# Kernel tuning notes

Hardware: AMD Instinct MI355X
Metric: run time of the kernel (lower is better)

## Reference

```python
import jax, jax.numpy as jnp
import numpy as np

L, D, H, F, NB = 6, 1024, 16, 4096, 33  # layers, d_model, heads, ffn_hidden, rel buckets
DH = D // H
B, S = 4, 1024


def _ln(x, g, b):
    m = x.mean(-1, keepdims=True)
    v = ((x - m) ** 2).mean(-1, keepdims=True)
    return (x - m) * jax.lax.rsqrt(v + 1e-6) * g + b


def setup_inputs() -> dict:
    key = jax.random.key(0)
    ks = iter(jax.random.split(key, 16))
    nrm = lambda shape, s: jax.random.normal(next(ks), shape, jnp.float32) * s
    w = 0.02
    return {
        "x": jax.random.normal(next(ks), (B, S, D), jnp.float32),
        "relative_ids": jax.random.randint(next(ks), (S, S), 0, NB, jnp.int32),
        "Wq": nrm((L, D, D), w), "bq": jnp.zeros((L, D)),
        "Wk": nrm((L, D, D), w), "bk": jnp.zeros((L, D)),
        "Wv": nrm((L, D, D), w), "bv": jnp.zeros((L, D)),
        "Wo": nrm((L, D, D), w), "bo": jnp.zeros((L, D)),
        "Erel": nrm((L, NB, DH), w),          # relative key embeddings (rel-e)
        "Brel": nrm((L, H, NB), w),           # relative bias per head (rel-b)
        "g1": jnp.ones((L, D)), "be1": jnp.zeros((L, D)),
        "g2": jnp.ones((L, D)), "be2": jnp.zeros((L, D)),
        "W1": nrm((L, D, F), w), "b1": jnp.zeros((L, F)),
        "W2": nrm((L, F, D), w), "b2": jnp.zeros((L, D)),
    }


def reference(x, relative_ids, Wq, bq, Wk, bk, Wv, bv, Wo, bo, Erel, Brel,
              g1, be1, g2, be2, W1, b1, W2, b2):
    scale = 1.0 / np.sqrt(DH).astype(np.float32)
    for l in range(L):
        # --- relative-position MHA (rel-eb) ---
        q = (x @ Wq[l] + bq[l]).reshape(B, S, H, DH).transpose(0, 2, 1, 3)
        k = (x @ Wk[l] + bk[l]).reshape(B, S, H, DH).transpose(0, 2, 1, 3)
        v = (x @ Wv[l] + bv[l]).reshape(B, S, H, DH).transpose(0, 2, 1, 3)
        scores = jnp.einsum('bhqd,bhkd->bhqk', q, k)
        e = Erel[l][relative_ids]                      # [S,S,DH]
        scores = scores + jnp.einsum('bhqd,qkd->bhqk', q, e)
        scores = scores + Brel[l][:, relative_ids][None]  # [1,H,S,S]
        attn = jax.nn.softmax(scores * scale, axis=-1)
        a = jnp.einsum('bhqk,bhkd->bqhd', attn, v).reshape(B, S, D)
        a = a @ Wo[l] + bo[l]
        # dropout p=0.1 is identity in eval mode
        ff_in = _ln(x + a, g1[l], be1[l])
        ff = jax.nn.relu(ff_in @ W1[l] + b1[l]) @ W2[l] + b2[l]
        x = _ln(ff_in + ff, g2[l], be2[l])
    return x
```

## Files before the change

kernel.cpp:

```cpp
#include <hip/hip_runtime.h>

typedef __attribute__((ext_vector_type(8))) short short8;
typedef __attribute__((ext_vector_type(4))) float f32x4;
typedef __attribute__((ext_vector_type(4))) unsigned short ushort4v;

#define AS1(p) ((const __attribute__((address_space(1))) void*)(p))
#define AS3(p) ((__attribute__((address_space(3))) void*)(p))

__device__ __forceinline__ float bf2f(unsigned short v) {
    union { unsigned u; float f; } c; c.u = ((unsigned)v) << 16; return c.f;
}
__device__ __forceinline__ unsigned short f2bf(float f) {
    union { float f; unsigned u; } c; c.f = f;
    unsigned u = c.u;
    return (unsigned short)((u + 0x7FFFu + ((u >> 16) & 1u)) >> 16);
}

__global__ __launch_bounds__(256) void transpose_cvt(
    const float* __restrict__ in, unsigned short* __restrict__ out, int R, int C)
{
    __shared__ float tile[64][68];
    int bx = blockIdx.x * 64;
    int by = blockIdx.y * 64;
    int tx = threadIdx.x & 15, ty = threadIdx.x >> 4;
    #pragma unroll
    for (int i = 0; i < 4; i++) {
        int r = ty + i * 16;
        f32x4 v = *(const f32x4*)(in + (size_t)(by + r) * C + bx + tx * 4);
        *(f32x4*)&tile[r][tx * 4] = v;
    }
    __syncthreads();
    #pragma unroll
    for (int i = 0; i < 4; i++) {
        int c = ty + i * 16;
        ushort4v o = { f2bf(tile[tx * 4 + 0][c]), f2bf(tile[tx * 4 + 1][c]),
                       f2bf(tile[tx * 4 + 2][c]), f2bf(tile[tx * 4 + 3][c]) };
        *(ushort4v*)(out + (size_t)(bx + c) * R + by + tx * 4) = o;
    }
}

__global__ __launch_bounds__(256) void cvt_f32_bf16(
    const float* __restrict__ in, unsigned short* __restrict__ out, int n)
{
    int i4 = (blockIdx.x * 256 + threadIdx.x) * 4;
    if (i4 < n) {
        f32x4 v = *(const f32x4*)(in + i4);
        ushort4v o = { f2bf(v[0]), f2bf(v[1]), f2bf(v[2]), f2bf(v[3]) };
        *(ushort4v*)(out + i4) = o;
    }
}

__global__ __launch_bounds__(256) void transpose_v(
    const unsigned short* __restrict__ in, unsigned short* __restrict__ out)
{
    __shared__ unsigned short t[64][66];
    int bh = blockIdx.y, s0 = blockIdx.x * 64;
    int tid = threadIdx.x;
    int r = tid >> 2, c = (tid & 3) * 16;
    const unsigned short* ip = in + ((size_t)bh * 1024 + s0 + r) * 64 + c;
    short8 a0 = *(const short8*)ip;
    short8 a1 = *(const short8*)(ip + 8);
    #pragma unroll
    for (int i = 0; i < 8; i++) t[r][c + i] = (unsigned short)a0[i];
    #pragma unroll
    for (int i = 0; i < 8; i++) t[r][c + 8 + i] = (unsigned short)a1[i];
    __syncthreads();
    int d = tid >> 2, sc = (tid & 3) * 16;
    short8 v0, v1;
    #pragma unroll
    for (int i = 0; i < 8; i++) v0[i] = (short)t[sc + i][d];
    #pragma unroll
    for (int i = 0; i < 8; i++) v1[i] = (short)t[sc + 8 + i][d];
    unsigned short* op = out + ((size_t)bh * 64 + d) * 1024 + s0 + sc;
    *(short8*)op = v0;
    *(short8*)(op + 8) = v1;
}

template <int MODE>
__global__ __launch_bounds__(256)
void gemm_bt(const unsigned short* __restrict__ A,
             const unsigned short* __restrict__ Bt,
             const float* __restrict__ bias0,
             const float* __restrict__ bias1,
             const float* __restrict__ bias2,
             float* __restrict__ outF0,
             float* __restrict__ outF1,
             float* __restrict__ outF2,
             float* __restrict__ outF3,
             unsigned short* __restrict__ outB,
             int M, int N, int K, int Kc)
{
    __shared__ __align__(16) unsigned short As[2][128 * 32];
    __shared__ __align__(16) unsigned short Bs[2][128 * 32];

    int tid = threadIdx.x;
    int wave = tid >> 6, lane = tid & 63;
    int ml = lane & 15, quad = lane >> 4;

    int nx = gridDim.x, ny = gridDim.y;
    int nwg = nx * ny;
    int lin = blockIdx.x + nx * (blockIdx.y + ny * blockIdx.z);
    int total = nwg * gridDim.z;
    int cpx = total >> 3;
    int logical = (lin & 7) * cpx + (lin >> 3);
    int z = logical / nwg;
    int rem = logical - z * nwg;
    int m0 = (rem / nx) * 128, n0 = (rem % nx) * 128;

    int wm = (wave >> 1) * 64, wn = (wave & 1) * 64;

    f32x4 acc[4][4];
    #pragma unroll
    for (int i = 0; i < 4; i++)
        #pragma unroll
        for (int j = 0; j < 4; j++)
            #pragma unroll
            for (int r = 0; r < 4; r++) acc[i][j][r] = 0.0f;

    int srow = lane >> 2, skp = (lane & 3) * 8;
    int kbeg = z * Kc;
    int nt = Kc >> 5;

    auto stage = [&](int buf, int k0) {
        #pragma unroll
        for (int c2 = 0; c2 < 2; c2++) {
            int c = wave + c2 * 4;
            const unsigned short* ga = A + (size_t)(m0 + c * 16 + srow) * K + (k0 + skp);
            __builtin_amdgcn_global_load_lds(AS1(ga), AS3(&As[buf][c * 512]), 16, 0, 0);
            const unsigned short* gb = Bt + (size_t)(n0 + c * 16 + srow) * K + (k0 + skp);
            __builtin_amdgcn_global_load_lds(AS1(gb), AS3(&Bs[buf][c * 512]), 16, 0, 0);
        }
    };

    stage(0, kbeg);
    __syncthreads();

    for (int t = 0; t < nt; t++) {
        int cur = t & 1;
        if (t + 1 < nt) stage(cur ^ 1, kbeg + (t + 1) * 32);

        short8 af[4], bfr[4];
        #pragma unroll
        for (int i = 0; i < 4; i++)
            af[i] = *(const short8*)(&As[cur][(wm + i * 16 + ml) * 32 + quad * 8]);
        #pragma unroll
        for (int j = 0; j < 4; j++)
            bfr[j] = *(const short8*)(&Bs[cur][(wn + j * 16 + ml) * 32 + quad * 8]);
        #pragma unroll
        for (int i = 0; i < 4; i++)
            #pragma unroll
            for (int j = 0; j < 4; j++)
                acc[i][j] = __builtin_amdgcn_mfma_f32_16x16x32_bf16(af[i], bfr[j], acc[i][j], 0, 0, 0);

        if (t + 1 < nt) __syncthreads();
    }

    float* outF = (z == 0) ? outF0 : (z == 1) ? outF1 : (z == 2) ? outF2 : outF3;

    size_t Ns = (size_t)N;
    #pragma unroll
    for (int j = 0; j < 4; j++) {
        int ng = n0 + wn + j * 16 + ml;
        float bv;
        if (MODE == 2) {
            int which = ng >> 10;
            const float* bp = (which == 0) ? bias0 : ((which == 1) ? bias1 : bias2);
            bv = bp[ng & 1023];
        } else {
            bv = (z == 0) ? bias0[ng] : 0.0f;
        }
        #pragma unroll
        for (int i = 0; i < 4; i++) {
            #pragma unroll
            for (int r = 0; r < 4; r++) {
                int mg = m0 + wm + i * 16 + quad * 4 + r;
                float v = acc[i][j][r] + bv;
                if (MODE == 0) {
                    outF[(size_t)mg * Ns + ng] = v;
                } else if (MODE == 1) {
                    outB[(size_t)mg * Ns + ng] = f2bf(fmaxf(v, 0.0f));
                } else {
                    int which = ng >> 10, wi = ng & 1023;
                    int h = wi >> 6, d = wi & 63;
                    int b = mg >> 10, s = mg & 1023;
                    outB[(size_t)which * 4194304 +
                         ((size_t)(b * 16 + h) * 1024 + s) * 64 + d] = f2bf(v);
                }
            }
        }
    }
}

__global__ __launch_bounds__(256) void qe_kernel(
    const unsigned short* __restrict__ q,
    const float* __restrict__ Erel,
    const float* __restrict__ Brel,
    float* __restrict__ out)
{
    int idx = blockIdx.x * 256 + threadIdx.x;
    if (idx >= 2162688) return;
    int n = idx % 33;
    int row = idx / 33;
    const short8* qv = (const short8*)(q + (size_t)row * 64);
    float s = 0.0f;
    #pragma unroll
    for (int c = 0; c < 8; c++) {
        short8 qq = qv[c];
        const float* e = Erel + n * 64 + c * 8;
        #pragma unroll
        for (int j = 0; j < 8; j++) s += bf2f((unsigned short)qq[j]) * e[j];
    }
    int h = (row >> 10) & 15;
    out[idx] = (s + Brel[h * 33 + n]) * 0.125f;
}

__global__ __launch_bounds__(256, 3)
void attn_kernel(const unsigned short* __restrict__ Q,
                 const unsigned short* __restrict__ Kin,
                 const unsigned short* __restrict__ Vt,
                 const int* __restrict__ rid,
                 const float* __restrict__ qEc,
                 unsigned short* __restrict__ outp)
{
    const float scale = 0.125f;
    int bid = blockIdx.x;
    int bh = bid & 63, qt = bid >> 6;
    int b = bh >> 4, h = bh & 15;
    int q0 = qt * 64;
    size_t bhs = (size_t)bh;

    __shared__ __align__(16) unsigned short Ks[64 * 72];
    __shared__ __align__(16) unsigned short VT[64 * 72];
    __shared__ __align__(16) unsigned short Ps[4][16 * 72];
    __shared__ float combS[4][528];

    int tid = threadIdx.x;
    int wave = tid >> 6, lane = tid & 63;
    int ml = lane & 15, quad = lane >> 4;

    const unsigned short* Qp = Q + (bhs * 1024 + q0) * 64;
    const unsigned short* Kp = Kin + bhs * 65536;
    const unsigned short* Vp = Vt + bhs * 65536;

    short8 aq0 = *(const short8*)(Qp + (size_t)(wave * 16 + ml) * 64 + quad * 8);
    short8 aq1 = *(const short8*)(Qp + (size_t)(wave * 16 + ml) * 64 + 32 + quad * 8);

    {
        const float* qEw = qEc + (bhs * 1024 + q0 + wave * 16) * 33;
        for (int i = lane; i < 528; i += 64) combS[wave][i] = qEw[i];
    }

    int srow = tid >> 2, scol = (tid & 3) * 16;
    const unsigned short* Kg = Kp + (size_t)srow * 64 + scol;
    const unsigned short* Vg = Vp + (size_t)srow * 1024 + scol;
    const int* ridBase = rid + (size_t)(q0 + wave * 16 + quad * 4) * 1024;

    float m_st[4], l_st[4];
    f32x4 o_acc[4];
    #pragma unroll
    for (int r = 0; r < 4; r++) { m_st[r] = -1e30f; l_st[r] = 0.0f; }
    #pragma unroll
    for (int j = 0; j < 4; j++)
        #pragma unroll
        for (int r = 0; r < 4; r++) o_acc[j][r] = 0.0f;

    short8 pk0 = *(const short8*)(Kg);
    short8 pk1 = *(const short8*)(Kg + 8);
    short8 pv0 = *(const short8*)(Vg);
    short8 pv1 = *(const short8*)(Vg + 8);

    for (int kt = 0; kt < 16; kt++) {
        if (kt > 0) __syncthreads();
        *(short8*)(Ks + srow * 72 + scol)     = pk0;
        *(short8*)(Ks + srow * 72 + scol + 8) = pk1;
        *(short8*)(VT + srow * 72 + scol)     = pv0;
        *(short8*)(VT + srow * 72 + scol + 8) = pv1;
        __syncthreads();

        if (kt + 1 < 16) {
            pk0 = *(const short8*)(Kg + (kt + 1) * 4096);
            pk1 = *(const short8*)(Kg + (kt + 1) * 4096 + 8);
            pv0 = *(const short8*)(Vg + (kt + 1) * 64);
            pv1 = *(const short8*)(Vg + (kt + 1) * 64 + 8);
        }

        int rv[4][4];
        #pragma unroll
        for (int r = 0; r < 4; r++) {
            const int* rp = ridBase + (size_t)r * 1024 + kt * 64 + ml;
            #pragma unroll
            for (int j = 0; j < 4; j++) rv[r][j] = rp[j * 16];
        }

        f32x4 s_acc[4];
        #pragma unroll
        for (int j = 0; j < 4; j++)
            #pragma unroll
            for (int r = 0; r < 4; r++) s_acc[j][r] = 0.0f;
        __builtin_amdgcn_s_setprio(1);
        #pragma unroll
        for (int j = 0; j < 4; j++) {
            short8 bk0 = *(const short8*)(Ks + (j * 16 + ml) * 72 + quad * 8);
            short8 bk1 = *(const short8*)(Ks + (j * 16 + ml) * 72 + 32 + quad * 8);
            s_acc[j] = __builtin_amdgcn_mfma_f32_16x16x32_bf16(aq0, bk0, s_acc[j], 0, 0, 0);
            s_acc[j] = __builtin_amdgcn_mfma_f32_16x16x32_bf16(aq1, bk1, s_acc[j], 0, 0, 0);
        }
        __builtin_amdgcn_s_setprio(0);

        float mxl[4];
        #pragma unroll
        for (int r = 0; r < 4; r++) {
            int rl = quad * 4 + r;
            #pragma unroll
            for (int j = 0; j < 4; j++)
                s_acc[j][r] = s_acc[j][r] * scale + combS[wave][rl * 33 + rv[r][j]];
            mxl[r] = fmaxf(fmaxf(s_acc[0][r], s_acc[1][r]), fmaxf(s_acc[2][r], s_acc[3][r]));
        }

        bool ok = (mxl[0] <= m_st[0] + 8.0f) & (mxl[1] <= m_st[1] + 8.0f)
                & (mxl[2] <= m_st[2] + 8.0f) & (mxl[3] <= m_st[3] + 8.0f);
        if (__all(ok)) {
            #pragma unroll
            for (int r = 0; r < 4; r++) {
                int rl = quad * 4 + r;
                float ps = 0.0f;
                #pragma unroll
                for (int j = 0; j < 4; j++) {
                    float pv = __expf(s_acc[j][r] - m_st[r]);
                    ps += pv;
                    Ps[wave][rl * 72 + j * 16 + ml] = f2bf(pv);
                }
                l_st[r] += ps;
            }
        } else {
            #pragma unroll
            for (int r = 0; r < 4; r++) {
                int rl = quad * 4 + r;
                float m0 = mxl[r];
                m0 = fmaxf(m0, __shfl_xor(m0, 1, 64));
                m0 = fmaxf(m0, __shfl_xor(m0, 2, 64));
                m0 = fmaxf(m0, __shfl_xor(m0, 4, 64));
                m0 = fmaxf(m0, __shfl_xor(m0, 8, 64));
                float mnew = fmaxf(m_st[r], m0);
                float alpha = __expf(m_st[r] - mnew);
                float ps = 0.0f;
                #pragma unroll
                for (int j = 0; j < 4; j++) {
                    float pv = __expf(s_acc[j][r] - mnew);
                    ps += pv;
                    Ps[wave][rl * 72 + j * 16 + ml] = f2bf(pv);
                }
                l_st[r] = l_st[r] * alpha + ps;
                m_st[r] = mnew;
                #pragma unroll
                for (int j = 0; j < 4; j++) o_acc[j][r] *= alpha;
            }
        }

        short8 ap0 = *(const short8*)(&Ps[wave][ml * 72 + quad * 8]);
        short8 ap1 = *(const short8*)(&Ps[wave][ml * 72 + 32 + quad * 8]);
        __builtin_amdgcn_s_setprio(1);
        #pragma unroll
        for (int j = 0; j < 4; j++) {
            short8 bv0 = *(const short8*)(VT + (j * 16 + ml) * 72 + quad * 8);
            short8 bv1 = *(const short8*)(VT + (j * 16 + ml) * 72 + 32 + quad * 8);
            o_acc[j] = __builtin_amdgcn_mfma_f32_16x16x32_bf16(ap0, bv0, o_acc[j], 0, 0, 0);
            o_acc[j] = __builtin_amdgcn_mfma_f32_16x16x32_bf16(ap1, bv1, o_acc[j], 0, 0, 0);
        }
        __builtin_amdgcn_s_setprio(0);
    }

    #pragma unroll
    for (int r = 0; r < 4; r++) {
        float lr = l_st[r];
        lr += __shfl_xor(lr, 1, 64);
        lr += __shfl_xor(lr, 2, 64);
        lr += __shfl_xor(lr, 4, 64);
        lr += __shfl_xor(lr, 8, 64);
        int qrow = wave * 16 + quad * 4 + r;
        float invl = 1.0f / lr;
        size_t base = ((size_t)(b * 1024 + q0 + qrow)) * 1024 + h * 64;
        #pragma unroll
        for (int j = 0; j < 4; j++)
            outp[base + j * 16 + ml] = f2bf(o_acc[j][r] * invl);
    }
}

template <int NP>
__global__ __launch_bounds__(256) void ln_kernel(
    const float* __restrict__ a,
    const float* __restrict__ p0, const float* __restrict__ p1,
    const float* __restrict__ p2, const float* __restrict__ p3,
    const float* __restrict__ g, const float* __restrict__ be,
    float* __restrict__ outF, unsigned short* __restrict__ outB)
{
    int row = blockIdx.x, tid = threadIdx.x;
    int wave = tid >> 6, lane = tid & 63;
    size_t off = (size_t)row * 1024 + tid * 4;
    f32x4 x = *(const f32x4*)(a + off);
    {
        f32x4 t = *(const f32x4*)(p0 + off);
        #pragma unroll
        for (int i = 0; i < 4; i++) x[i] += t[i];
    }
    if (NP > 1) {
        f32x4 t = *(const f32x4*)(p1 + off);
        #pragma unroll
        for (int i = 0; i < 4; i++) x[i] += t[i];
    }
    if (NP > 2) {
        f32x4 t = *(const f32x4*)(p2 + off);
        #pragma unroll
        for (int i = 0; i < 4; i++) x[i] += t[i];
    }
    if (NP > 3) {
        f32x4 t = *(const f32x4*)(p3 + off);
        #pragma unroll
        for (int i = 0; i < 4; i++) x[i] += t[i];
    }
    float s1 = x[0] + x[1] + x[2] + x[3];
    float s2 = x[0]*x[0] + x[1]*x[1] + x[2]*x[2] + x[3]*x[3];
    #pragma unroll
    for (int offx = 1; offx < 64; offx <<= 1) {
        s1 += __shfl_xor(s1, offx, 64);
        s2 += __shfl_xor(s2, offx, 64);
    }
    __shared__ float r1[4], r2[4];
    if (lane == 0) { r1[wave] = s1; r2[wave] = s2; }
    __syncthreads();
    s1 = r1[0] + r1[1] + r1[2] + r1[3];
    s2 = r2[0] + r2[1] + r2[2] + r2[3];
    float mean = s1 * (1.0f / 1024.0f);
    float var  = s2 * (1.0f / 1024.0f) - mean * mean;
    float inv  = rsqrtf(var + 1e-6f);
    f32x4 gg = *(const f32x4*)(g + tid * 4);
    f32x4 bb = *(const f32x4*)(be + tid * 4);
    f32x4 o;
    #pragma unroll
    for (int i = 0; i < 4; i++) o[i] = (x[i] - mean) * inv * gg[i] + bb[i];
    *(f32x4*)(outF + off) = o;
    if (outB != nullptr) {
        ushort4v ov = { f2bf(o[0]), f2bf(o[1]), f2bf(o[2]), f2bf(o[3]) };
        *(ushort4v*)(outB + off) = ov;
    }
}

extern "C" void kernel_launch(void* const* d_in, const int* in_sizes, int n_in,
                              void* d_out, int out_size, void* d_ws, size_t ws_size,
                              hipStream_t stream)
{
    const float* x_in = (const float*)d_in[0];
    const int*   rid  = (const int*)d_in[1];
    const float* Wq = (const float*)d_in[2];  const float* bq = (const float*)d_in[3];
    const float* Wk = (const float*)d_in[4];  const float* bk = (const float*)d_in[5];
    const float* Wv = (const float*)d_in[6];  const float* bv = (const float*)d_in[7];
    const float* Wo = (const float*)d_in[8];  const float* bo = (const float*)d_in[9];
    const float* Erel = (const float*)d_in[10];
    const float* Brel = (const float*)d_in[11];
    const float* g1 = (const float*)d_in[12]; const float* be1 = (const float*)d_in[13];
    const float* g2 = (const float*)d_in[14]; const float* be2 = (const float*)d_in[15];
    const float* W1 = (const float*)d_in[16]; const float* b1 = (const float*)d_in[17];
    const float* W2 = (const float*)d_in[18]; const float* b2 = (const float*)d_in[19];

    char* p = (char*)d_ws;
    auto alloc = [&](size_t bytes) {
        char* r = p; p += (bytes + 255) & ~(size_t)255; return (void*)r;
    };
    unsigned short* wqkv_t = (unsigned short*)alloc(3ull * 1024 * 1024 * 2);
    unsigned short* wo_t   = (unsigned short*)alloc(1024ull * 1024 * 2);
    unsigned short* w1_t   = (unsigned short*)alloc(4096ull * 1024 * 2);
    unsigned short* w2_t   = (unsigned short*)alloc(1024ull * 4096 * 2);
    float*          xf     = (float*)alloc(4096ull * 1024 * 4);
    unsigned short* xb     = (unsigned short*)alloc(4096ull * 1024 * 2);
    unsigned short* qkvb   = (unsigned short*)alloc(3ull * 4194304 * 2);
    unsigned short* vtb    = (unsigned short*)alloc(4194304ull * 2);
    unsigned short* attnb  = (unsigned short*)alloc(4096ull * 1024 * 2);
    float*          qEcb   = (float*)alloc(2162688ull * 4);
    float*          proj   = (float*)alloc(4096ull * 1024 * 4);
    float*          ffin   = (float*)alloc(4096ull * 1024 * 4);
    unsigned short* ffinb  = (unsigned short*)alloc(4096ull * 1024 * 2);
    unsigned short* hb     = qkvb;

    float* pP2 = (float*)attnb;
    float* pP3 = (float*)wqkv_t;

    cvt_f32_bf16<<<4096, 256, 0, stream>>>(x_in, xb, 4194304);

    const float* xcur = x_in;
    for (int l = 0; l < 6; l++) {
        transpose_cvt<<<dim3(16, 16), 256, 0, stream>>>(Wq + (size_t)l * 1048576, wqkv_t,           1024, 1024);
        transpose_cvt<<<dim3(16, 16), 256, 0, stream>>>(Wk + (size_t)l * 1048576, wqkv_t + 1048576, 1024, 1024);
        transpose_cvt<<<dim3(16, 16), 256, 0, stream>>>(Wv + (size_t)l * 1048576, wqkv_t + 2097152, 1024, 1024);
        transpose_cvt<<<dim3(16, 16), 256, 0, stream>>>(Wo + (size_t)l * 1048576, wo_t,             1024, 1024);
        transpose_cvt<<<dim3(64, 16), 256, 0, stream>>>(W1 + (size_t)l * 4194304, w1_t, 1024, 4096);
        transpose_cvt<<<dim3(16, 64), 256, 0, stream>>>(W2 + (size_t)l * 4194304, w2_t, 4096, 1024);

        gemm_bt<2><<<dim3(24, 32, 1), 256, 0, stream>>>(
            xb, wqkv_t, bq + l * 1024, bk + l * 1024, bv + l * 1024,
            nullptr, nullptr, nullptr, nullptr, qkvb, 4096, 3072, 1024, 1024);

        transpose_v<<<dim3(16, 64), 256, 0, stream>>>(qkvb + 8388608, vtb);

        qe_kernel<<<8448, 256, 0, stream>>>(qkvb, Erel + l * 2112, Brel + l * 528, qEcb);

        attn_kernel<<<1024, 256, 0, stream>>>(
            qkvb, qkvb + 4194304, vtb, rid, qEcb, attnb);

        gemm_bt<0><<<dim3(8, 32, 2), 256, 0, stream>>>(
            attnb, wo_t, bo + l * 1024, nullptr, nullptr,
            proj, ffin, nullptr, nullptr, nullptr, 4096, 1024, 1024, 512);

        ln_kernel<2><<<4096, 256, 0, stream>>>(
            xcur, proj, ffin, nullptr, nullptr,
            g1 + l * 1024, be1 + l * 1024, ffin, ffinb);

        gemm_bt<1><<<dim3(32, 32, 1), 256, 0, stream>>>(
            ffinb, w1_t, b1 + l * 4096, nullptr, nullptr,
            nullptr, nullptr, nullptr, nullptr, hb, 4096, 4096, 1024, 1024);

        gemm_bt<0><<<dim3(8, 32, 4), 256, 0, stream>>>(
            hb, w2_t, b2 + l * 1024, nullptr, nullptr,
            proj, xf, pP2, pP3, nullptr, 4096, 1024, 4096, 1024);

        float* lnout = (l == 5) ? (float*)d_out : xf;
        unsigned short* lnoutb = (l == 5) ? nullptr : xb;
        ln_kernel<4><<<4096, 256, 0, stream>>>(
            ffin, proj, xf, pP2, pP3,
            g2 + l * 1024, be2 + l * 1024, lnout, lnoutb);
        xcur = xf;
    }
}
```

Measured before the change: 2.272 ms.

## Compute q·Erel bucket scores with MFMA tiles instead of scalar dot products

```diff
diff --git a/kernel.cpp b/kernel.cpp
--- a/kernel.cpp
+++ b/kernel.cpp
@@ -197,21 +197,69 @@
     const float* __restrict__ Brel,
     float* __restrict__ out)
 {
-    int idx = blockIdx.x * 256 + threadIdx.x;
-    if (idx >= 2162688) return;
-    int n = idx % 33;
-    int row = idx / 33;
-    const short8* qv = (const short8*)(q + (size_t)row * 64);
-    float s = 0.0f;
-    #pragma unroll
-    for (int c = 0; c < 8; c++) {
-        short8 qq = qv[c];
-        const float* e = Erel + n * 64 + c * 8;
-        #pragma unroll
-        for (int j = 0; j < 8; j++) s += bf2f((unsigned short)qq[j]) * e[j];
-    }
-    int h = (row >> 10) & 15;
-    out[idx] = (s + Brel[h * 33 + n]) * 0.125f;
+    __shared__ __align__(16) unsigned short El[48 * 72];
+    __shared__ float brS[33];
+
+    int tid = threadIdx.x;
+    int blk = blockIdx.x;
+    int h = (blk >> 3) & 15;
+
+    for (int i = tid; i < 15 * 72; i += 256) El[33 * 72 + i] = 0;
+    for (int i = tid; i < 2112; i += 256) {
+        int n = i >> 6, k = i & 63;
+        El[n * 72 + k] = f2bf(Erel[i]);
+    }
+    if (tid < 33) brS[tid] = Brel[h * 33 + tid];
+    __syncthreads();
+
+    int wave = tid >> 6, lane = tid & 63;
+    int ml = lane & 15, quad = lane >> 4;
+
+    const unsigned short* qp = q + ((size_t)blk * 128 + wave * 32) * 64;
+    short8 a0[2], a1[2];
+    #pragma unroll
+    for (int i = 0; i < 2; i++) {
+        a0[i] = *(const short8*)(qp + (size_t)(i * 16 + ml) * 64 + quad * 8);
+        a1[i] = *(const short8*)(qp + (size_t)(i * 16 + ml) * 64 + 32 + quad * 8);
+    }
+    short8 b0[3], b1[3];
+    #pragma unroll
+    for (int j = 0; j < 3; j++) {
+        b0[j] = *(const short8*)(El + (j * 16 + ml) * 72 + quad * 8);
+        b1[j] = *(const short8*)(El + (j * 16 + ml) * 72 + 32 + quad * 8);
+    }
+
+    f32x4 acc[2][3];
+    #pragma unroll
+    for (int i = 0; i < 2; i++)
+        #pragma unroll
+        for (int j = 0; j < 3; j++)
+            #pragma unroll
+            for (int r = 0; r < 4; r++) acc[i][j][r] = 0.0f;
+
+    #pragma unroll
+    for (int i = 0; i < 2; i++)
+        #pragma unroll
+        for (int j = 0; j < 3; j++) {
+            acc[i][j] = __builtin_amdgcn_mfma_f32_16x16x32_bf16(a0[i], b0[j], acc[i][j], 0, 0, 0);
+            acc[i][j] = __builtin_amdgcn_mfma_f32_16x16x32_bf16(a1[i], b1[j], acc[i][j], 0, 0, 0);
+        }
+
+    #pragma unroll
+    for (int j = 0; j < 3; j++) {
+        int n = j * 16 + ml;
+        if (n < 33) {
+            float bn = brS[n];
+            #pragma unroll
+            for (int i = 0; i < 2; i++) {
+                #pragma unroll
+                for (int r = 0; r < 4; r++) {
+                    size_t row = (size_t)blk * 128 + wave * 32 + i * 16 + quad * 4 + r;
+                    out[row * 33 + n] = (acc[i][j][r] + bn) * 0.125f;
+                }
+            }
+        }
+    }
 }
 
 __global__ __launch_bounds__(256, 3)
@@ -501,7 +549,7 @@
 
         transpose_v<<<dim3(16, 64), 256, 0, stream>>>(qkvb + 8388608, vtb);
 
-        qe_kernel<<<8448, 256, 0, stream>>>(qkvb, Erel + l * 2112, Brel + l * 528, qEcb);
+        qe_kernel<<<512, 256, 0, stream>>>(qkvb, Erel + l * 2112, Brel + l * 528, qEcb);
 
         attn_kernel<<<1024, 256, 0, stream>>>(
             qkvb, qkvb + 4194304, vtb, rid, qEcb, attnb);
```

Result: faster. 1.937 ms (-14.7%).
